# Performance work log

Measured on AMD Instinct MI355X. Metric: run time of the kernel, lower is better.

Reference implementation:

```python
import jax, jax.numpy as jnp
import numpy as np

N_NODES = 100000
N_EDGES = 1600000
IN_CH = 128
OUT_CH = 128


def setup_inputs() -> dict:
    key = jax.random.key(0)
    k1, k2, k3 = jax.random.split(key, 3)
    x = jax.random.normal(k1, (N_NODES, IN_CH), dtype=jnp.float32)
    edge_index = jax.random.randint(k2, (2, N_EDGES), 0, N_NODES, dtype=jnp.int64)
    # glorot-like init for the linear weight, stored as [in, out]
    W = jax.random.normal(k3, (IN_CH, OUT_CH), dtype=jnp.float32) * (2.0 / (IN_CH + OUT_CH)) ** 0.5
    bias = jnp.zeros((OUT_CH,), dtype=jnp.float32)
    return {"x": x, "edge_index": edge_index, "W": W, "bias": bias}


def reference(x, edge_index, W, bias):
    N = x.shape[0]
    # linear transform (bias-free, matches Linear(in, out, bias=False))
    h = x @ W  # [N, out]

    # add self loops (improved=False -> fill_value = 1.0)
    loop = jnp.arange(N, dtype=edge_index.dtype)
    src = jnp.concatenate([edge_index[0], loop])
    dst = jnp.concatenate([edge_index[1], loop])
    ew = jnp.ones(src.shape[0], dtype=h.dtype)  # edge_weight None -> ones

    # symmetric GCN normalization: deg from dst, norm = d^-1/2[src] * w * d^-1/2[dst]
    deg = jax.ops.segment_sum(ew, dst, num_segments=N)
    deg_inv_sqrt = jnp.where(deg > 0, jax.lax.rsqrt(deg), 0.0)
    w = deg_inv_sqrt[src] * ew * deg_inv_sqrt[dst]

    # spmm aggregation: out[dst] += w * h[src]
    out = jax.ops.segment_sum(h[src] * w[:, None], dst, num_segments=N)
    return out + bias
```

## Files before the change

kernel.cpp:

```cpp
#include <hip/hip_runtime.h>
#include <hip/hip_bf16.h>

constexpr int kNodes = 100000;
constexpr int kEdges = 1600000;
constexpr int kCh    = 128;
constexpr int kCap   = 64;
constexpr int kPartSize = kNodes / 8;
constexpr int kPartBlocks = 1024;
constexpr int kZeroBlocks = (kNodes + 255) / 256;

typedef __attribute__((ext_vector_type(8))) short short8;
typedef __attribute__((ext_vector_type(4))) float floatx4;


__global__ __launch_bounds__(256) void k_prep(const float* __restrict__ W,
                                              short8* __restrict__ WtF,
                                              int* __restrict__ cnt) {
  if (blockIdx.x < 8) {
    int e = blockIdx.x * 256 + threadIdx.x;
    int lane = e & 63;
    int c = (e >> 6) & 3;
    int t = e >> 8;
    int quad = lane >> 4;
    int mcol = lane & 15;
    short8 v;
    #pragma unroll
    for (int j = 0; j < 8; j++) {
      __hip_bfloat16 h = __float2bfloat16(W[(c * 32 + quad * 8 + j) * kCh + t * 16 + mcol]);
      v[j] = *(short*)&h;
    }
    WtF[e] = v;
  } else {
    int i = (blockIdx.x - 8) * 256 + threadIdx.x;
    if (i < kNodes) cnt[i] = 0;
  }
}


__global__ __launch_bounds__(256) void k_fill_bucket(const int* __restrict__ srcArr,
                                                     const int* __restrict__ dstArr,
                                                     int* __restrict__ cnt,
                                                     int* __restrict__ bucket) {
  int part = blockIdx.x & 7;
  int bip  = blockIdx.x >> 3;
  int lo = part * kPartSize;
  for (int e = bip * 256 + threadIdx.x; e < kEdges; e += (kPartBlocks >> 3) * 256) {
    int d = dstArr[e];
    if ((unsigned)(d - lo) < (unsigned)kPartSize) {
      int pos = atomicAdd(&cnt[d], 1);
      if (pos < kCap) bucket[(long)d * kCap + pos] = srcArr[e];
    }
  }
}


__global__ __launch_bounds__(512) void k_gemm_mfma(const float* __restrict__ x,
                                                   const short8* __restrict__ WtF,
                                                   const int* __restrict__ cnt,
                                                   __hip_bfloat16* __restrict__ hs) {
  __shared__ short8 Bf[2048];
  {
    const uint4* wsrc = (const uint4*)WtF;
    uint4* wdst = (uint4*)Bf;
    for (int i = threadIdx.x; i < 2048; i += 512) wdst[i] = wsrc[i];
  }
  __syncthreads();

  int wave = threadIdx.x >> 6;
  int lane = threadIdx.x & 63;
  int quad = lane >> 4;
  int mcol = lane & 15;
  long rowBase = ((long)blockIdx.x * 8 + wave) * 16;
  if (rowBase >= kNodes) return;

  float dnv[4];
  #pragma unroll
  for (int i = 0; i < 4; i++) {
    long r = rowBase + quad * 4 + i;
    if (r >= kNodes) r = kNodes - 1;
    dnv[i] = rsqrtf((float)(cnt[r] + 1));
  }

  long arow = rowBase + mcol;
  if (arow >= kNodes) arow = kNodes - 1;
  const float* xp = x + arow * kCh;
  short8 afrag[4];
  #pragma unroll
  for (int c = 0; c < 4; c++) {
    const float4* p = (const float4*)(xp + c * 32 + quad * 8);
    float4 v0 = p[0], v1 = p[1];
    float f[8] = {v0.x, v0.y, v0.z, v0.w, v1.x, v1.y, v1.z, v1.w};
    #pragma unroll
    for (int j = 0; j < 8; j++) {
      __hip_bfloat16 h = __float2bfloat16(f[j]);
      afrag[c][j] = *(short*)&h;
    }
  }

  #pragma unroll
  for (int t = 0; t < 8; t++) {
    floatx4 acc = {0.f, 0.f, 0.f, 0.f};
    #pragma unroll
    for (int c = 0; c < 4; c++) {
      short8 b = Bf[(t * 4 + c) * 64 + lane];
      acc = __builtin_amdgcn_mfma_f32_16x16x32_bf16(afrag[c], b, acc, 0, 0, 0);
    }
    #pragma unroll
    for (int i = 0; i < 4; i++) {
      long r = rowBase + quad * 4 + i;
      if (r < kNodes) {
        hs[r * kCh + t * 16 + mcol] = __float2bfloat16(acc[i] * dnv[i]);
      }
    }
  }
}


__global__ __launch_bounds__(256) void k_aggregate(const int* __restrict__ cnt,
                                                   const int* __restrict__ bucket,
                                                   const __hip_bfloat16* __restrict__ hs,
                                                   const float* __restrict__ bias,
                                                   float* __restrict__ out) {
  int gid  = blockIdx.x * 256 + threadIdx.x;
  int node = gid >> 6;
  int lane = gid & 63;
  if (node >= kNodes) return;

  const __hip_bfloat162* hbase = (const __hip_bfloat162*)hs;

  float2 sf = __bfloat1622float2(hbase[(long)node * (kCh / 2) + lane]);
  float acc0 = sf.x;
  float acc1 = sf.y;

  int degRaw = cnt[node];
  int c = degRaw < kCap ? degRaw : kCap;
  const int* bkt = bucket + (long)node * kCap;

  int j = 0;
  for (; j + 7 < c; j += 8) {
    int s[8];
    #pragma unroll
    for (int u = 0; u < 8; u++) s[u] = bkt[j + u];
    __hip_bfloat162 v[8];
    #pragma unroll
    for (int u = 0; u < 8; u++) v[u] = hbase[(long)s[u] * (kCh / 2) + lane];
    #pragma unroll
    for (int u = 0; u < 8; u++) {
      float2 f = __bfloat1622float2(v[u]);
      acc0 += f.x;
      acc1 += f.y;
    }
  }
  for (; j < c; ++j) {
    float2 f = __bfloat1622float2(hbase[(long)bkt[j] * (kCh / 2) + lane]);
    acc0 += f.x;
    acc1 += f.y;
  }

  float dd = rsqrtf((float)(degRaw + 1));
  float2 b = ((const float2*)bias)[lane];
  float2 o;
  o.x = dd * acc0 + b.x;
  o.y = dd * acc1 + b.y;
  ((float2*)(out + (long)node * kCh))[lane] = o;
}


extern "C" void kernel_launch(void* const* d_in, const int* in_sizes, int n_in,
                              void* d_out, int out_size, void* d_ws, size_t ws_size,
                              hipStream_t stream) {
  const float* x    = (const float*)d_in[0];
  const int*   ei   = (const int*)d_in[1];
  const float* W    = (const float*)d_in[2];
  const float* bias = (const float*)d_in[3];
  float* out = (float*)d_out;

  const int* srcArr = ei;
  const int* dstArr = ei + kEdges;

  char* ws = (char*)d_ws;
  size_t off = 0;
  __hip_bfloat16* hs = (__hip_bfloat16*)(ws + off); off += (size_t)kNodes * kCh * 2;
  int*   bucket  = (int*)  (ws + off); off += (size_t)kNodes * kCap * 4;
  short8* WtF    = (short8*)(ws + off); off += (size_t)kCh * kCh * 2;
  int*   cnt     = (int*)  (ws + off); off += (size_t)kNodes * 4;

  k_prep<<<8 + kZeroBlocks, 256, 0, stream>>>(W, WtF, cnt);

  k_fill_bucket<<<kPartBlocks, 256, 0, stream>>>(srcArr, dstArr, cnt, bucket);

  int gGemm = (kNodes + 127) / 128;
  k_gemm_mfma<<<gGemm, 512, 0, stream>>>(x, WtF, cnt, hs);

  long aggThreads = (long)kNodes * 64;
  int gAgg = (int)((aggThreads + 255) / 256);
  k_aggregate<<<gAgg, 256, 0, stream>>>(cnt, bucket, hs, bias, out);
}
```

Before: 265.1 us.

## Fuse bucket fill and GEMM into one launch, move src normalization to aggregation

Merges the bucket-fill and the MFMA GEMM into a single kernel whose blocks are split by index, so the two independent stages can overlap on the GPU. Since the GEMM no longer has to wait for degree counts, the source-side deg^-1/2 scaling moves into the aggregate kernel, which gathers cnt[src] for every neighbor. The weight fragment conversion now runs inside each GEMM block, cnt is zeroed with hipMemsetAsync, and dst indices are read as vector4 nontemporal loads. The cost is an extra random cnt gather plus an rsqrt per edge in aggregation, and the W conversion is repeated in every GEMM block.

```diff
diff --git a/kernel.cpp b/kernel.cpp
--- a/kernel.cpp
+++ b/kernel.cpp
@@ -6,63 +6,52 @@
 constexpr int kCh    = 128;
 constexpr int kCap   = 64;
 constexpr int kPartSize = kNodes / 8;
-constexpr int kPartBlocks = 1024;
-constexpr int kZeroBlocks = (kNodes + 255) / 256;
+constexpr int kFillBlocks = 512;
+constexpr int kGemmBlocks = (kNodes + 127) / 128;
 
 typedef __attribute__((ext_vector_type(8))) short short8;
 typedef __attribute__((ext_vector_type(4))) float floatx4;
+typedef __attribute__((ext_vector_type(4))) int   intx4;
 
 
-__global__ __launch_bounds__(256) void k_prep(const float* __restrict__ W,
-                                              short8* __restrict__ WtF,
-                                              int* __restrict__ cnt) {
-  if (blockIdx.x < 8) {
-    int e = blockIdx.x * 256 + threadIdx.x;
-    int lane = e & 63;
-    int c = (e >> 6) & 3;
-    int t = e >> 8;
-    int quad = lane >> 4;
-    int mcol = lane & 15;
+__global__ __launch_bounds__(512) void k_fused(const float* __restrict__ x,
+                                               const float* __restrict__ W,
+                                               const int* __restrict__ srcArr,
+                                               const int* __restrict__ dstArr,
+                                               int* __restrict__ cnt,
+                                               int* __restrict__ bucket,
+                                               __hip_bfloat16* __restrict__ hs) {
+  if (blockIdx.x < kFillBlocks) {
+    int part = blockIdx.x & 7;
+    int bip  = blockIdx.x >> 3;
+    int lo = part * kPartSize;
+    const intx4* d4 = (const intx4*)dstArr;
+    for (int i = bip * 512 + (int)threadIdx.x; i < kEdges / 4; i += (kFillBlocks >> 3) * 512) {
+      intx4 dv = __builtin_nontemporal_load(d4 + i);
+      #pragma unroll
+      for (int k = 0; k < 4; k++) {
+        int d = dv[k];
+        if ((unsigned)(d - lo) < (unsigned)kPartSize) {
+          int s = srcArr[4 * i + k];
+          int pos = atomicAdd(&cnt[d], 1);
+          if (pos < kCap) bucket[(long)d * kCap + pos] = s;
+        }
+      }
+    }
+    return;
+  }
+
+  __shared__ short8 Bf[2048];
+  for (int e = threadIdx.x; e < 2048; e += 512) {
+    int lane = e & 63, c = (e >> 6) & 3, tt = e >> 8;
+    int quad = lane >> 4, mcol = lane & 15;
     short8 v;
     #pragma unroll
     for (int j = 0; j < 8; j++) {
-      __hip_bfloat16 h = __float2bfloat16(W[(c * 32 + quad * 8 + j) * kCh + t * 16 + mcol]);
+      __hip_bfloat16 h = __float2bfloat16(W[(c * 32 + quad * 8 + j) * kCh + tt * 16 + mcol]);
       v[j] = *(short*)&h;
     }
-    WtF[e] = v;
-  } else {
-    int i = (blockIdx.x - 8) * 256 + threadIdx.x;
-    if (i < kNodes) cnt[i] = 0;
-  }
-}
-
-
-__global__ __launch_bounds__(256) void k_fill_bucket(const int* __restrict__ srcArr,
-                                                     const int* __restrict__ dstArr,
-                                                     int* __restrict__ cnt,
-                                                     int* __restrict__ bucket) {
-  int part = blockIdx.x & 7;
-  int bip  = blockIdx.x >> 3;
-  int lo = part * kPartSize;
-  for (int e = bip * 256 + threadIdx.x; e < kEdges; e += (kPartBlocks >> 3) * 256) {
-    int d = dstArr[e];
-    if ((unsigned)(d - lo) < (unsigned)kPartSize) {
-      int pos = atomicAdd(&cnt[d], 1);
-      if (pos < kCap) bucket[(long)d * kCap + pos] = srcArr[e];
-    }
-  }
-}
-
-
-__global__ __launch_bounds__(512) void k_gemm_mfma(const float* __restrict__ x,
-                                                   const short8* __restrict__ WtF,
-                                                   const int* __restrict__ cnt,
-                                                   __hip_bfloat16* __restrict__ hs) {
-  __shared__ short8 Bf[2048];
-  {
-    const uint4* wsrc = (const uint4*)WtF;
-    uint4* wdst = (uint4*)Bf;
-    for (int i = threadIdx.x; i < 2048; i += 512) wdst[i] = wsrc[i];
+    Bf[e] = v;
   }
   __syncthreads();
 
@@ -70,16 +59,9 @@
   int lane = threadIdx.x & 63;
   int quad = lane >> 4;
   int mcol = lane & 15;
-  long rowBase = ((long)blockIdx.x * 8 + wave) * 16;
+  int gb = blockIdx.x - kFillBlocks;
+  long rowBase = ((long)gb * 8 + wave) * 16;
   if (rowBase >= kNodes) return;
-
-  float dnv[4];
-  #pragma unroll
-  for (int i = 0; i < 4; i++) {
-    long r = rowBase + quad * 4 + i;
-    if (r >= kNodes) r = kNodes - 1;
-    dnv[i] = rsqrtf((float)(cnt[r] + 1));
-  }
 
   long arow = rowBase + mcol;
   if (arow >= kNodes) arow = kNodes - 1;
@@ -108,9 +90,7 @@
     #pragma unroll
     for (int i = 0; i < 4; i++) {
       long r = rowBase + quad * 4 + i;
-      if (r < kNodes) {
-        hs[r * kCh + t * 16 + mcol] = __float2bfloat16(acc[i] * dnv[i]);
-      }
+      if (r < kNodes) hs[r * kCh + t * 16 + mcol] = __float2bfloat16(acc[i]);
     }
   }
 }
@@ -128,11 +108,13 @@
 
   const __hip_bfloat162* hbase = (const __hip_bfloat162*)hs;
 
+  int degRaw = cnt[node];
+  float dd = rsqrtf((float)(degRaw + 1));
+
   float2 sf = __bfloat1622float2(hbase[(long)node * (kCh / 2) + lane]);
-  float acc0 = sf.x;
-  float acc1 = sf.y;
+  float acc0 = dd * sf.x;
+  float acc1 = dd * sf.y;
 
-  int degRaw = cnt[node];
   int c = degRaw < kCap ? degRaw : kCap;
   const int* bkt = bucket + (long)node * kCap;
 
@@ -141,23 +123,28 @@
     int s[8];
     #pragma unroll
     for (int u = 0; u < 8; u++) s[u] = bkt[j + u];
+    int cs[8];
+    #pragma unroll
+    for (int u = 0; u < 8; u++) cs[u] = cnt[s[u]];
     __hip_bfloat162 v[8];
     #pragma unroll
     for (int u = 0; u < 8; u++) v[u] = hbase[(long)s[u] * (kCh / 2) + lane];
     #pragma unroll
     for (int u = 0; u < 8; u++) {
+      float dv = rsqrtf((float)(cs[u] + 1));
       float2 f = __bfloat1622float2(v[u]);
-      acc0 += f.x;
-      acc1 += f.y;
+      acc0 = fmaf(dv, f.x, acc0);
+      acc1 = fmaf(dv, f.y, acc1);
     }
   }
   for (; j < c; ++j) {
-    float2 f = __bfloat1622float2(hbase[(long)bkt[j] * (kCh / 2) + lane]);
-    acc0 += f.x;
-    acc1 += f.y;
+    int s = bkt[j];
+    float dv = rsqrtf((float)(cnt[s] + 1));
+    float2 f = __bfloat1622float2(hbase[(long)s * (kCh / 2) + lane]);
+    acc0 = fmaf(dv, f.x, acc0);
+    acc1 = fmaf(dv, f.y, acc1);
   }
 
-  float dd = rsqrtf((float)(degRaw + 1));
   float2 b = ((const float2*)bias)[lane];
   float2 o;
   o.x = dd * acc0 + b.x;
@@ -182,15 +169,11 @@
   size_t off = 0;
   __hip_bfloat16* hs = (__hip_bfloat16*)(ws + off); off += (size_t)kNodes * kCh * 2;
   int*   bucket  = (int*)  (ws + off); off += (size_t)kNodes * kCap * 4;
-  short8* WtF    = (short8*)(ws + off); off += (size_t)kCh * kCh * 2;
   int*   cnt     = (int*)  (ws + off); off += (size_t)kNodes * 4;
 
-  k_prep<<<8 + kZeroBlocks, 256, 0, stream>>>(W, WtF, cnt);
+  (void)hipMemsetAsync(cnt, 0, (size_t)kNodes * sizeof(int), stream);
 
-  k_fill_bucket<<<kPartBlocks, 256, 0, stream>>>(srcArr, dstArr, cnt, bucket);
-
-  int gGemm = (kNodes + 127) / 128;
-  k_gemm_mfma<<<gGemm, 512, 0, stream>>>(x, WtF, cnt, hs);
+  k_fused<<<kFillBlocks + kGemmBlocks, 512, 0, stream>>>(x, W, srcArr, dstArr, cnt, bucket, hs);
 
   long aggThreads = (long)kNodes * 64;
   int gAgg = (int)((aggThreads + 255) / 256);
```

After: 283.2 us. 1.07x slower.
